# Optimization experiments

Measured on AMD Instinct MI355X. Metric: run time of the kernel, lower is better.

## Reference

```python
import jax, jax.numpy as jnp
import numpy as np

N = 100000
E = 1600000
F = 64
THETA = (0.6, -0.4, 0.3, -0.2, 0.1)  # k = 5 polynomial coefficients


def setup_inputs() -> dict:
    key = jax.random.key(0)
    kx, ke = jax.random.split(key)
    x = jax.random.normal(kx, (N, F), dtype=jnp.float32)
    edge_index = jax.random.randint(ke, (2, E), 0, N, dtype=jnp.int64)
    return {"x": x, "edge_index": edge_index}


def _l_sym_mul(feat, src, dst, deg_inv_sqrt, n):
    # L_sym * feat = feat - D^{-1/2} A D^{-1/2} feat
    src_norm = feat[src] * deg_inv_sqrt[src]            # [E, F] gather + scale
    agg = jax.ops.segment_sum(src_norm, dst, num_segments=n)  # scatter-add to dst
    return feat - deg_inv_sqrt * agg


def reference(x, edge_index):
    src, dst = edge_index[0], edge_index[1]
    n = x.shape[0]
    # in-degree from dst, clamp to >= 1, D^{-1/2} as [N, 1]
    deg = jax.ops.segment_sum(jnp.ones((src.shape[0],), dtype=x.dtype), dst,
                              num_segments=n)
    deg = jnp.maximum(deg, 1.0)[:, None]
    deg_inv_sqrt = deg ** -0.5

    h_acc = THETA[0] * x
    feat = x
    for k in range(1, len(THETA)):
        feat = _l_sym_mul(feat, src, dst, deg_inv_sqrt, n)
        h_acc = h_acc + THETA[k] * feat
    return h_acc
```

## Files before the change

### kernel.cpp

```cpp
#include <hip/hip_runtime.h>


constexpr int kF = 64;
constexpr int BSHIFT = 8;
constexpr int NB = 1 << BSHIFT;
constexpr int TILE = 2048;
constexpr int KMAX = 512;

static __device__ __forceinline__ float bfl(unsigned u) {
    return __uint_as_float(u << 16);
}
static __device__ __forceinline__ float bfh(unsigned u) {
    return __uint_as_float(u & 0xffff0000u);
}
static __device__ __forceinline__ unsigned f2bf(float f) {
    unsigned u = __float_as_uint(f);
    return (u + 0x7fffu + ((u >> 16) & 1u)) >> 16;
}
static __device__ __forceinline__ unsigned pack2(float a, float b) {
    return f2bf(a) | (f2bf(b) << 16);
}

__global__ void k_binA(const int* __restrict__ src, const int* __restrict__ dst,
                       unsigned* __restrict__ pairs, int* __restrict__ gcursor,
                       const float4* __restrict__ x4, uint4* __restrict__ xb4,
                       int n8, int E, int K, int cap) {
    __shared__ int hist[KMAX];
    __shared__ int gb[KMAX];
    const int tid = threadIdx.x;
    const long long tb = (long long)blockIdx.x * TILE;
    const int tcount = (int)min((long long)TILE, (long long)E - tb);

    {
        int per = (n8 + gridDim.x - 1) / (int)gridDim.x;
        int b0 = blockIdx.x * per;
        int b1 = min(b0 + per, n8);
        for (int i = b0 + tid; i < b1; i += 512) {
            float4 a = x4[2 * i];
            float4 b = x4[2 * i + 1];
            uint4 o;
            o.x = pack2(a.x, a.y);
            o.y = pack2(a.z, a.w);
            o.z = pack2(b.x, b.y);
            o.w = pack2(b.z, b.w);
            xb4[i] = o;
        }
    }

    hist[tid] = 0;
    __syncthreads();
    int dc[4], sc[4];
    #pragma unroll
    for (int k = 0; k < 4; ++k) {
        int i = tid + k * 512;
        if (i < tcount) {
            dc[k] = dst[tb + i];
            sc[k] = src[tb + i];
            atomicAdd(&hist[dc[k] >> BSHIFT], 1);
        } else {
            dc[k] = -1;
        }
    }
    __syncthreads();
    int hv = hist[tid];
    gb[tid] = (tid < K && hv > 0) ? atomicAdd(&gcursor[tid], hv) : 0;
    hist[tid] = 0;
    __syncthreads();
    #pragma unroll
    for (int k = 0; k < 4; ++k) {
        if (dc[k] >= 0) {
            int d = dc[k];
            int b = d >> BSHIFT;
            int pos = atomicAdd(&hist[b], 1);
            pairs[(size_t)b * cap + gb[b] + pos] =
                ((unsigned)(d & (NB - 1)) << 23) | (unsigned)sc[k];
        }
    }
}

__global__ void k_binB(const unsigned* __restrict__ pairs, const int* __restrict__ gcursor,
                       int* __restrict__ rp, float* __restrict__ dinv,
                       float* __restrict__ dinv2, float* __restrict__ rdeg,
                       int* __restrict__ csr, int N, int E, int K, int cap) {
    __shared__ int gsc[KMAX];
    __shared__ int cnt[NB];
    __shared__ int stmp[NB];
    __shared__ int cur[NB];
    const int b = blockIdx.x;
    const int tid = threadIdx.x;

    int gv = (tid < K) ? gcursor[tid] : 0;
    gsc[tid] = gv;
    __syncthreads();
    for (int o = 1; o < KMAX; o <<= 1) {
        int t = (tid >= o) ? gsc[tid - o] : 0;
        __syncthreads();
        gsc[tid] += t;
        __syncthreads();
    }
    const int ecnt = gcursor[b];
    const int base = gsc[b] - ecnt;
    const unsigned* bp = pairs + (size_t)b * cap;

    if (tid < NB) cnt[tid] = 0;
    __syncthreads();
    for (int i = tid; i < ecnt; i += 512)
        atomicAdd(&cnt[bp[i] >> 23], 1);
    __syncthreads();
    int v = (tid < NB) ? cnt[tid] : 0;
    if (tid < NB) stmp[tid] = v;
    __syncthreads();
    for (int o = 1; o < NB; o <<= 1) {
        int t = (tid >= o && tid < NB) ? stmp[tid - o] : 0;
        __syncthreads();
        if (tid < NB) stmp[tid] += t;
        __syncthreads();
    }
    int node = (b << BSHIFT) + tid;
    if (tid < NB) {
        int abs0 = base + stmp[tid] - v;
        cur[tid] = abs0;
        if (node < N) {
            rp[node] = abs0;
            float d = fmaxf((float)v, 1.0f);
            dinv[node]  = rsqrtf(d);
            dinv2[node] = 1.0f / d;
            rdeg[node]  = sqrtf(d);
        }
    }
    if (b == K - 1 && tid == 0) rp[N] = E;
    __syncthreads();
    for (int i = tid; i < ecnt; i += 512) {
        unsigned p = bp[i];
        int pos = atomicAdd(&cur[p >> 23], 1);
        csr[pos] = (int)(p & 0x7FFFFFu);
    }
}

__global__ void k_g0(const uint4* __restrict__ xb, const float* __restrict__ dinv,
                     uint4* __restrict__ g0, int n8) {
    int i = blockIdx.x * blockDim.x + threadIdx.x;
    if (i >= n8) return;
    float di = dinv[i >> 3];
    uint4 xv = xb[i];
    uint4 o;
    o.x = pack2(di * bfl(xv.x), di * bfh(xv.x));
    o.y = pack2(di * bfl(xv.y), di * bfh(xv.y));
    o.z = pack2(di * bfl(xv.z), di * bfh(xv.z));
    o.w = pack2(di * bfl(xv.w), di * bfh(xv.w));
    g0[i] = o;
}

__global__ void k_gather(const int* __restrict__ rp, const int* __restrict__ csr,
                         const unsigned short* __restrict__ gin,
                         const float* __restrict__ dinv2,
                         unsigned short* __restrict__ gout, int n) {
    int wid = (blockIdx.x * blockDim.x + threadIdx.x) >> 6;
    int lane = threadIdx.x & 63;
    int half = lane >> 5;
    int r = (lane >> 3) & 3;
    int c = lane & 7;
    int node = wid * 2 + half;
    if (wid * 2 >= n) return;
    bool valid = node < n;
    int beg = valid ? rp[node] : 0;
    int end = valid ? rp[node + 1] : 0;
    int len = end - beg;
    int olen = __shfl_xor(len, 32, 64);
    int mlen = (len > olen) ? len : olen;

    float acc[8] = {0.f, 0.f, 0.f, 0.f, 0.f, 0.f, 0.f, 0.f};
    for (int i = 0; i < mlen; i += 8) {
        int j1 = beg + i + r;
        int j2 = j1 + 4;
        bool ok1 = j1 < end;
        bool ok2 = j2 < end;
        int s1 = csr[ok1 ? j1 : 0];
        int s2 = csr[ok2 ? j2 : 0];
        float w1 = ok1 ? 1.0f : 0.0f;
        float w2 = ok2 ? 1.0f : 0.0f;
        uint4 ra = *(const uint4*)(gin + ((size_t)s1 << 6) + (c << 3));
        uint4 rb = *(const uint4*)(gin + ((size_t)s2 << 6) + (c << 3));
        acc[0] += w1 * bfl(ra.x); acc[1] += w1 * bfh(ra.x);
        acc[2] += w1 * bfl(ra.y); acc[3] += w1 * bfh(ra.y);
        acc[4] += w1 * bfl(ra.z); acc[5] += w1 * bfh(ra.z);
        acc[6] += w1 * bfl(ra.w); acc[7] += w1 * bfh(ra.w);
        acc[0] += w2 * bfl(rb.x); acc[1] += w2 * bfh(rb.x);
        acc[2] += w2 * bfl(rb.y); acc[3] += w2 * bfh(rb.y);
        acc[4] += w2 * bfl(rb.z); acc[5] += w2 * bfh(rb.z);
        acc[6] += w2 * bfl(rb.w); acc[7] += w2 * bfh(rb.w);
    }
    #pragma unroll
    for (int m = 8; m <= 16; m <<= 1) {
        #pragma unroll
        for (int i = 0; i < 8; ++i)
            acc[i] += __shfl_xor(acc[i], m, 64);
    }

    if (r == 0 && valid) {
        size_t off = ((size_t)node << 6) + (c << 3);
        uint4 rr = *(const uint4*)(gin + off);
        float d2 = dinv2[node];
        uint4 o;
        o.x = pack2(bfl(rr.x) - d2 * acc[0], bfh(rr.x) - d2 * acc[1]);
        o.y = pack2(bfl(rr.y) - d2 * acc[2], bfh(rr.y) - d2 * acc[3]);
        o.z = pack2(bfl(rr.z) - d2 * acc[4], bfh(rr.z) - d2 * acc[5]);
        o.w = pack2(bfl(rr.w) - d2 * acc[6], bfh(rr.w) - d2 * acc[7]);
        *(uint4*)(gout + off) = o;
    }
}

__global__ void k_final(const uint4* __restrict__ xb, const float* __restrict__ rdeg,
                        const uint4* __restrict__ g1, const uint4* __restrict__ g2,
                        const uint4* __restrict__ g3, const uint4* __restrict__ g4,
                        float4* __restrict__ h4, int n8,
                        float t0, float t1, float t2, float t3, float t4) {
    int i = blockIdx.x * blockDim.x + threadIdx.x;
    if (i >= n8) return;
    float rd = rdeg[i >> 3];
    float s1 = rd * t1, s2 = rd * t2, s3 = rd * t3, s4 = rd * t4;
    uint4 xv = xb[i];
    uint4 a = g1[i], b = g2[i], cc = g3[i], d = g4[i];
    float4 h0, h1;
    h0.x = t0 * bfl(xv.x) + s1 * bfl(a.x) + s2 * bfl(b.x) + s3 * bfl(cc.x) + s4 * bfl(d.x);
    h0.y = t0 * bfh(xv.x) + s1 * bfh(a.x) + s2 * bfh(b.x) + s3 * bfh(cc.x) + s4 * bfh(d.x);
    h0.z = t0 * bfl(xv.y) + s1 * bfl(a.y) + s2 * bfl(b.y) + s3 * bfl(cc.y) + s4 * bfl(d.y);
    h0.w = t0 * bfh(xv.y) + s1 * bfh(a.y) + s2 * bfh(b.y) + s3 * bfh(cc.y) + s4 * bfh(d.y);
    h1.x = t0 * bfl(xv.z) + s1 * bfl(a.z) + s2 * bfl(b.z) + s3 * bfl(cc.z) + s4 * bfl(d.z);
    h1.y = t0 * bfh(xv.z) + s1 * bfh(a.z) + s2 * bfh(b.z) + s3 * bfh(cc.z) + s4 * bfh(d.z);
    h1.z = t0 * bfl(xv.w) + s1 * bfl(a.w) + s2 * bfl(b.w) + s3 * bfl(cc.w) + s4 * bfl(d.w);
    h1.w = t0 * bfh(xv.w) + s1 * bfh(a.w) + s2 * bfh(b.w) + s3 * bfh(cc.w) + s4 * bfh(d.w);
    h4[2 * i] = h0;
    h4[2 * i + 1] = h1;
}

extern "C" void kernel_launch(void* const* d_in, const int* in_sizes, int n_in,
                              void* d_out, int out_size, void* d_ws, size_t ws_size,
                              hipStream_t stream) {
    const float* x  = (const float*)d_in[0];
    const int*   ei = (const int*)d_in[1];
    const int N = in_sizes[0] / kF;
    const int E = in_sizes[1] / 2;
    const int* src = ei;
    const int* dst = ei + E;
    float* h = (float*)d_out;

    const int K = (N + NB - 1) >> BSHIFT;
    const int cap = 2 * ((E + K - 1) / K);

    char* ws = (char*)d_ws;
    size_t off = 0;
    auto carve = [&](size_t bytes) {
        void* p = ws + off;
        off = (off + bytes + 511) & ~(size_t)511;
        return p;
    };
    int*            gcursor = (int*)carve((size_t)K * 4);
    int*            rp      = (int*)carve((size_t)(N + 1) * 4);
    float*          dinv    = (float*)carve((size_t)N * 4);
    float*          dinv2   = (float*)carve((size_t)N * 4);
    float*          rdeg    = (float*)carve((size_t)N * 4);
    int*            csr     = (int*)carve((size_t)E * 4);
    unsigned short* xb      = (unsigned short*)carve((size_t)N * kF * 2);
    unsigned short* g0      = (unsigned short*)carve((size_t)N * kF * 2);
    unsigned short* g1      = (unsigned short*)carve((size_t)N * kF * 2);
    unsigned short* g2      = (unsigned short*)carve((size_t)N * kF * 2);
    unsigned short* g3      = (unsigned short*)carve((size_t)N * kF * 2);
    unsigned short* g4      = (unsigned short*)carve((size_t)N * kF * 2);
    unsigned*       pairs   = (unsigned*)g4;

    const float theta[5] = {0.6f, -0.4f, 0.3f, -0.2f, 0.1f};
    const int n8 = N * kF / 8;

    hipMemsetAsync(gcursor, 0, (size_t)K * 4, stream);
    k_binA<<<(E + TILE - 1) / TILE, 512, 0, stream>>>(src, dst, pairs, gcursor,
                                                      (const float4*)x, (uint4*)xb,
                                                      n8, E, K, cap);
    k_binB<<<K, 512, 0, stream>>>(pairs, gcursor, rp, dinv, dinv2, rdeg, csr,
                                  N, E, K, cap);
    k_g0<<<(n8 + 255) / 256, 256, 0, stream>>>((const uint4*)xb, dinv, (uint4*)g0, n8);

    const int nwaves = (N + 1) / 2;
    const int gblocks = (nwaves + 3) / 4;
    k_gather<<<gblocks, 256, 0, stream>>>(rp, csr, g0, dinv2, g1, N);
    k_gather<<<gblocks, 256, 0, stream>>>(rp, csr, g1, dinv2, g2, N);
    k_gather<<<gblocks, 256, 0, stream>>>(rp, csr, g2, dinv2, g3, N);
    k_gather<<<gblocks, 256, 0, stream>>>(rp, csr, g3, dinv2, g4, N);

    k_final<<<(n8 + 255) / 256, 256, 0, stream>>>((const uint4*)xb, rdeg,
                                                  (const uint4*)g1, (const uint4*)g2,
                                                  (const uint4*)g3, (const uint4*)g4,
                                                  (float4*)h, n8,
                                                  theta[0], theta[1], theta[2],
                                                  theta[3], theta[4]);
}
```

Measured before the change: 267.2 us.

## Fuse g0 scaling into binB and software-pipeline gather loads

Folds the k_g0 kernel into k_binB: each bin block keeps its nodes' D^-1/2 in shared memory and scales its own slice of x into g0. This drops one kernel launch and the dinv global array. The gather loop is also software-pipelined, so CSR indices are prefetched two iterations ahead and feature rows one iteration ahead, overlapping index loads with row loads. The cost is more registers per thread, which may lower occupancy in the four gather passes.

```diff
diff --git a/kernel.cpp b/kernel.cpp
--- a/kernel.cpp
+++ b/kernel.cpp
@@ -79,13 +79,15 @@
 }
 
 __global__ void k_binB(const unsigned* __restrict__ pairs, const int* __restrict__ gcursor,
-                       int* __restrict__ rp, float* __restrict__ dinv,
-                       float* __restrict__ dinv2, float* __restrict__ rdeg,
-                       int* __restrict__ csr, int N, int E, int K, int cap) {
+                       int* __restrict__ rp, float* __restrict__ dinv2,
+                       float* __restrict__ rdeg, int* __restrict__ csr,
+                       const uint4* __restrict__ xb, uint4* __restrict__ g0,
+                       int N, int E, int K, int cap) {
     __shared__ int gsc[KMAX];
     __shared__ int cnt[NB];
     __shared__ int stmp[NB];
     __shared__ int cur[NB];
+    __shared__ float sdinv[NB];
     const int b = blockIdx.x;
     const int tid = threadIdx.x;
 
@@ -120,10 +122,10 @@
     if (tid < NB) {
         int abs0 = base + stmp[tid] - v;
         cur[tid] = abs0;
+        float d = fmaxf((float)v, 1.0f);
+        sdinv[tid] = rsqrtf(d);
         if (node < N) {
             rp[node] = abs0;
-            float d = fmaxf((float)v, 1.0f);
-            dinv[node]  = rsqrtf(d);
             dinv2[node] = 1.0f / d;
             rdeg[node]  = sqrtf(d);
         }
@@ -135,20 +137,20 @@
         int pos = atomicAdd(&cur[p >> 23], 1);
         csr[pos] = (int)(p & 0x7FFFFFu);
     }
-}
-
-__global__ void k_g0(const uint4* __restrict__ xb, const float* __restrict__ dinv,
-                     uint4* __restrict__ g0, int n8) {
-    int i = blockIdx.x * blockDim.x + threadIdx.x;
-    if (i >= n8) return;
-    float di = dinv[i >> 3];
-    uint4 xv = xb[i];
-    uint4 o;
-    o.x = pack2(di * bfl(xv.x), di * bfh(xv.x));
-    o.y = pack2(di * bfl(xv.y), di * bfh(xv.y));
-    o.z = pack2(di * bfl(xv.z), di * bfh(xv.z));
-    o.w = pack2(di * bfl(xv.w), di * bfh(xv.w));
-    g0[i] = o;
+    const int nbase = b << BSHIFT;
+    const int qmax = min(NB, N - nbase) << 3;
+    const uint4* xbp = xb + ((size_t)nbase << 3);
+    uint4* g0p = g0 + ((size_t)nbase << 3);
+    for (int q = tid; q < qmax; q += 512) {
+        float di = sdinv[q >> 3];
+        uint4 xv = xbp[q];
+        uint4 o;
+        o.x = pack2(di * bfl(xv.x), di * bfh(xv.x));
+        o.y = pack2(di * bfl(xv.y), di * bfh(xv.y));
+        o.z = pack2(di * bfl(xv.z), di * bfh(xv.z));
+        o.w = pack2(di * bfl(xv.w), di * bfh(xv.w));
+        g0p[q] = o;
+    }
 }
 
 __global__ void k_gather(const int* __restrict__ rp, const int* __restrict__ csr,
@@ -170,25 +172,49 @@
     int mlen = (len > olen) ? len : olen;
 
     float acc[8] = {0.f, 0.f, 0.f, 0.f, 0.f, 0.f, 0.f, 0.f};
+
+    uint4 rc1 = make_uint4(0, 0, 0, 0), rc2 = make_uint4(0, 0, 0, 0);
+    float wc1 = 0.f, wc2 = 0.f;
+    int sn1 = 0, sn2 = 0;
+    float wn1 = 0.f, wn2 = 0.f;
+    if (mlen > 0) {
+        int j1 = beg + r, j2 = j1 + 4;
+        bool o1 = j1 < end, o2 = j2 < end;
+        int s1 = csr[o1 ? j1 : 0];
+        int s2 = csr[o2 ? j2 : 0];
+        wc1 = o1 ? 1.f : 0.f;
+        wc2 = o2 ? 1.f : 0.f;
+        rc1 = *(const uint4*)(gin + ((size_t)s1 << 6) + (c << 3));
+        rc2 = *(const uint4*)(gin + ((size_t)s2 << 6) + (c << 3));
+        int j1b = beg + 8 + r, j2b = j1b + 4;
+        bool vb = 8 < mlen;
+        bool b1 = vb && (j1b < end), b2 = vb && (j2b < end);
+        sn1 = csr[b1 ? j1b : 0];
+        sn2 = csr[b2 ? j2b : 0];
+        wn1 = b1 ? 1.f : 0.f;
+        wn2 = b2 ? 1.f : 0.f;
+    }
     for (int i = 0; i < mlen; i += 8) {
-        int j1 = beg + i + r;
-        int j2 = j1 + 4;
-        bool ok1 = j1 < end;
-        bool ok2 = j2 < end;
-        int s1 = csr[ok1 ? j1 : 0];
-        int s2 = csr[ok2 ? j2 : 0];
-        float w1 = ok1 ? 1.0f : 0.0f;
-        float w2 = ok2 ? 1.0f : 0.0f;
-        uint4 ra = *(const uint4*)(gin + ((size_t)s1 << 6) + (c << 3));
-        uint4 rb = *(const uint4*)(gin + ((size_t)s2 << 6) + (c << 3));
-        acc[0] += w1 * bfl(ra.x); acc[1] += w1 * bfh(ra.x);
-        acc[2] += w1 * bfl(ra.y); acc[3] += w1 * bfh(ra.y);
-        acc[4] += w1 * bfl(ra.z); acc[5] += w1 * bfh(ra.z);
-        acc[6] += w1 * bfl(ra.w); acc[7] += w1 * bfh(ra.w);
-        acc[0] += w2 * bfl(rb.x); acc[1] += w2 * bfh(rb.x);
-        acc[2] += w2 * bfl(rb.y); acc[3] += w2 * bfh(rb.y);
-        acc[4] += w2 * bfl(rb.z); acc[5] += w2 * bfh(rb.z);
-        acc[6] += w2 * bfl(rb.w); acc[7] += w2 * bfh(rb.w);
+        uint4 rn1 = *(const uint4*)(gin + ((size_t)sn1 << 6) + (c << 3));
+        uint4 rn2 = *(const uint4*)(gin + ((size_t)sn2 << 6) + (c << 3));
+        int j1n = beg + i + 16 + r, j2n = j1n + 4;
+        bool vn = (i + 16) < mlen;
+        bool t1 = vn && (j1n < end), t2 = vn && (j2n < end);
+        int st1 = csr[t1 ? j1n : 0];
+        int st2 = csr[t2 ? j2n : 0];
+        float wt1 = t1 ? 1.f : 0.f, wt2 = t2 ? 1.f : 0.f;
+        acc[0] += wc1 * bfl(rc1.x); acc[1] += wc1 * bfh(rc1.x);
+        acc[2] += wc1 * bfl(rc1.y); acc[3] += wc1 * bfh(rc1.y);
+        acc[4] += wc1 * bfl(rc1.z); acc[5] += wc1 * bfh(rc1.z);
+        acc[6] += wc1 * bfl(rc1.w); acc[7] += wc1 * bfh(rc1.w);
+        acc[0] += wc2 * bfl(rc2.x); acc[1] += wc2 * bfh(rc2.x);
+        acc[2] += wc2 * bfl(rc2.y); acc[3] += wc2 * bfh(rc2.y);
+        acc[4] += wc2 * bfl(rc2.z); acc[5] += wc2 * bfh(rc2.z);
+        acc[6] += wc2 * bfl(rc2.w); acc[7] += wc2 * bfh(rc2.w);
+        rc1 = rn1; rc2 = rn2;
+        wc1 = wn1; wc2 = wn2;
+        sn1 = st1; sn2 = st2;
+        wn1 = wt1; wn2 = wt2;
     }
     #pragma unroll
     for (int m = 8; m <= 16; m <<= 1) {
@@ -257,7 +283,6 @@
     };
     int*            gcursor = (int*)carve((size_t)K * 4);
     int*            rp      = (int*)carve((size_t)(N + 1) * 4);
-    float*          dinv    = (float*)carve((size_t)N * 4);
     float*          dinv2   = (float*)carve((size_t)N * 4);
     float*          rdeg    = (float*)carve((size_t)N * 4);
     int*            csr     = (int*)carve((size_t)E * 4);
@@ -276,9 +301,8 @@
     k_binA<<<(E + TILE - 1) / TILE, 512, 0, stream>>>(src, dst, pairs, gcursor,
                                                       (const float4*)x, (uint4*)xb,
                                                       n8, E, K, cap);
-    k_binB<<<K, 512, 0, stream>>>(pairs, gcursor, rp, dinv, dinv2, rdeg, csr,
-                                  N, E, K, cap);
-    k_g0<<<(n8 + 255) / 256, 256, 0, stream>>>((const uint4*)xb, dinv, (uint4*)g0, n8);
+    k_binB<<<K, 512, 0, stream>>>(pairs, gcursor, rp, dinv2, rdeg, csr,
+                                  (const uint4*)xb, (uint4*)g0, N, E, K, cap);
 
     const int nwaves = (N + 1) / 2;
     const int gblocks = (nwaves + 3) / 4;
```

After: 253.5 us. 5.1% less time.
